# Kernel tuning notes

Measured on AMD Instinct MI355X. Metric: run time of the kernel, lower is better.

The kernel has to match this reference:

```python
import jax, jax.numpy as jnp
import numpy as np
import math

D_MODEL = 1024
N_HEADS = 16
D_HEAD = D_MODEL // N_HEADS
D_FF = 4 * D_MODEL
EPS = 1e-5


def layer_norm(x, gamma, beta):
    mu = jnp.mean(x, axis=-1, keepdims=True)
    var = jnp.var(x, axis=-1, keepdims=True)
    return (x - mu) * jax.lax.rsqrt(var + EPS) * gamma + beta


def setup_inputs() -> dict:
    key = jax.random.key(0)
    ks = jax.random.split(key, 8)
    B, C, D = 32, 256, D_MODEL
    s = 0.02
    return {
        "X": jax.random.normal(ks[0], (B, C, D), dtype=jnp.float32),
        "W_qkv": jax.random.normal(ks[1], (D, 3 * D), dtype=jnp.float32) * s,
        "b_qkv": jnp.zeros((3 * D,), dtype=jnp.float32),
        "W_proj": jax.random.normal(ks[2], (D, D), dtype=jnp.float32) * s,
        "b_proj": jnp.zeros((D,), dtype=jnp.float32),
        "g1": jnp.ones((D,), dtype=jnp.float32),
        "beta1": jnp.zeros((D,), dtype=jnp.float32),
        "g2": jnp.ones((D,), dtype=jnp.float32),
        "beta2": jnp.zeros((D,), dtype=jnp.float32),
        "W_ff1": jax.random.normal(ks[3], (D, D_FF), dtype=jnp.float32) * s,
        "b_ff1": jnp.zeros((D_FF,), dtype=jnp.float32),
        "W_ff2": jax.random.normal(ks[4], (D_FF, D), dtype=jnp.float32) * s,
        "b_ff2": jnp.zeros((D,), dtype=jnp.float32),
    }


def reference(X, W_qkv, b_qkv, W_proj, b_proj, g1, beta1, g2, beta2,
              W_ff1, b_ff1, W_ff2, b_ff2):
    B, C, D = X.shape
    H, Dh = N_HEADS, D_HEAD
    scale = 1.0 / math.sqrt(Dh)

    Xn = layer_norm(X, g1, beta1)
    qkv = Xn @ W_qkv + b_qkv                       # [B, C, 3D]
    q, k, v = jnp.split(qkv, 3, axis=-1)
    # split heads -> [B, H, C, Dh]
    sh = lambda t: t.reshape(B, C, H, Dh).transpose(0, 2, 1, 3)
    q, k, v = sh(q), sh(k), sh(v)

    scores = jnp.einsum("bhcd,bhkd->bhck", q, k) * scale  # [B, H, C, C]
    attn = jax.nn.softmax(scores, axis=-1)
    ctx = jnp.einsum("bhck,bhkd->bhcd", attn, v)           # [B, H, C, Dh]
    ctx = ctx.transpose(0, 2, 1, 3).reshape(B, C, D)

    X1 = X + (ctx @ W_proj + b_proj)
    X2n = layer_norm(X1, g2, beta2)
    h = jax.nn.gelu(X2n @ W_ff1 + b_ff1, approximate=False)
    X_out = X1 + (h @ W_ff2 + b_ff2)
    A = attn.mean(axis=1)                                   # [B, C, C]
    return (X_out, A)
```

## Files before the change

### kernel.cpp

```cpp
#include <hip/hip_runtime.h>
#include <cstdint>
#include <cstddef>

typedef short bf16x8 __attribute__((ext_vector_type(8)));
typedef float f32x4 __attribute__((ext_vector_type(4)));
typedef unsigned short u16;
typedef u16 u16x8 __attribute__((ext_vector_type(8)));

#define GLD16(gptr, lptr)                                                            \
  __builtin_amdgcn_global_load_lds((const __attribute__((address_space(1))) void*)(gptr), \
                                   (__attribute__((address_space(3))) void*)(lptr), 16, 0, 0)

__device__ __forceinline__ u16 f2bf(float f) {
  union { float f; unsigned u; } v; v.f = f;
  unsigned r = v.u + 0x7FFF + ((v.u >> 16) & 1);
  return (u16)(r >> 16);
}
__device__ __forceinline__ float bf2f(u16 h) {
  union { unsigned u; float f; } v; v.u = ((unsigned)h) << 16;
  return v.f;
}

__device__ __forceinline__ bf16x8 lds_read_sw64(const u16* base, int row, int col) {
  int byt = row * 128 + col * 2;
  byt ^= (row & 7) << 4;
  return *(const bf16x8*)((const char*)base + byt);
}

__global__ __launch_bounds__(256) void transpose_cast(const float* __restrict__ in,
                                                      u16* __restrict__ out, int R, int C) {
  __shared__ float tile[32][33];
  const int tx = threadIdx.x, ty = threadIdx.y;
  const int c0 = blockIdx.x * 32, r0 = blockIdx.y * 32;
#pragma unroll
  for (int i = 0; i < 32; i += 8)
    tile[ty + i][tx] = in[(size_t)(r0 + ty + i) * C + c0 + tx];
  __syncthreads();
#pragma unroll
  for (int i = 0; i < 32; i += 8)
    out[(size_t)(c0 + ty + i) * R + r0 + tx] = f2bf(tile[tx][ty + i]);
}

__global__ __launch_bounds__(256) void layernorm_bf16(const float* __restrict__ X,
                                                      const float* __restrict__ g,
                                                      const float* __restrict__ be,
                                                      u16* __restrict__ out) {
  const int row = blockIdx.x, t = threadIdx.x;
  const int lane = t & 63, wave = t >> 6;
  const float* x = X + (size_t)row * 1024;
  __shared__ float part[4];
  float v[4]; float s = 0.f;
#pragma unroll
  for (int i = 0; i < 4; ++i) { v[i] = x[t + i * 256]; s += v[i]; }
#pragma unroll
  for (int o = 32; o >= 1; o >>= 1) s += __shfl_xor(s, o);
  if (lane == 0) part[wave] = s;
  __syncthreads();
  const float mu = (part[0] + part[1] + part[2] + part[3]) * (1.f / 1024.f);
  float d2 = 0.f;
#pragma unroll
  for (int i = 0; i < 4; ++i) { float d = v[i] - mu; d2 += d * d; }
#pragma unroll
  for (int o = 32; o >= 1; o >>= 1) d2 += __shfl_xor(d2, o);
  __syncthreads();
  if (lane == 0) part[wave] = d2;
  __syncthreads();
  const float var = (part[0] + part[1] + part[2] + part[3]) * (1.f / 1024.f);
  const float rstd = rsqrtf(var + 1e-5f);
#pragma unroll
  for (int i = 0; i < 4; ++i) {
    const int c = t + i * 256;
    out[(size_t)row * 1024 + c] = f2bf((v[i] - mu) * rstd * g[c] + be[c]);
  }
}

template <int EPI, int WM, int WN, int BN>
__global__ __launch_bounds__(512, 2) void gemm_r2(const u16* __restrict__ A,
                                                  const u16* __restrict__ Bt,
                                                  const float* __restrict__ bias,
                                                  const float* __restrict__ res,
                                                  float* __restrict__ outf,
                                                  u16* __restrict__ outb,
                                                  int M, int N, int K) {
  constexpr int BM = 256;
  constexpr int WR = BM / WM, WC = BN / WN;
  constexpr int MF = WR / 16, NF = WC / 16;
  constexpr int ABYT = BM * 128, BBYT = BN * 128;
  constexpr int LA = BM / 64, LB = BN / 64;
  __shared__ __attribute__((aligned(16))) char lds[2 * (ABYT + BBYT)];

  const int t = threadIdx.x, lane = t & 63, wave = t >> 6;
  const int wm = wave / WN, wn = wave % WN;
  const int l15 = lane & 15, l16 = lane >> 4;

  const int lb = (blockIdx.x & 7) * ((int)gridDim.x >> 3) + ((int)blockIdx.x >> 3);
  const int NBN = N / BN;
  const int bm = (lb / NBN) * BM, bn = (lb % NBN) * BN;

  const u16* aptr[LA];
  const u16* bptr[LB];
#pragma unroll
  for (int c = 0; c < LA; ++c) {
    int Lb = c * 8192 + t * 16;
    int x = (Lb ^ ((Lb >> 3) & 0x70)) >> 1;
    aptr[c] = A + (size_t)(bm + (x >> 6)) * K + (x & 63);
  }
#pragma unroll
  for (int c = 0; c < LB; ++c) {
    int Lb = c * 8192 + t * 16;
    int x = (Lb ^ ((Lb >> 3) & 0x70)) >> 1;
    bptr[c] = Bt + (size_t)(bn + (x >> 6)) * K + (x & 63);
  }

  auto stage = [&](int p) {
    const int ko = p * 64;
    const int s = p & 1;
    char* ab = lds + s * ABYT + t * 16;
    char* bb = lds + 2 * ABYT + s * BBYT + t * 16;
#pragma unroll
    for (int c = 0; c < LA; ++c) GLD16(aptr[c] + ko, ab + c * 8192);
#pragma unroll
    for (int c = 0; c < LB; ++c) GLD16(bptr[c] + ko, bb + c * 8192);
  };
  stage(0);

  const int co0 = l16 * 16, co1 = 64 + l16 * 16;
  f32x4 acc[MF][NF] = {};
  const int nkt = K >> 6;

#pragma unroll 1
  for (int kt = 0; kt < nkt; ++kt) {
    asm volatile("s_waitcnt vmcnt(0)" ::: "memory");
    asm volatile("s_waitcnt lgkmcnt(0)" ::: "memory");
    asm volatile("s_barrier" ::: "memory");
    if (kt + 1 < nkt) stage(kt + 1);

    const int s = kt & 1;
    const char* ab = lds + s * ABYT;
    const char* bb = lds + 2 * ABYT + s * BBYT;
#pragma unroll
    for (int ks = 0; ks < 2; ++ks) {
      const int co = ks ? co1 : co0;
      bf16x8 a[MF], b[NF];
#pragma unroll
      for (int m = 0; m < MF; ++m) {
        const int r = wm * WR + m * 16 + l15;
        a[m] = *(const bf16x8*)(ab + r * 128 + (co ^ ((r & 7) << 4)));
      }
#pragma unroll
      for (int n = 0; n < NF; ++n) {
        const int r = wn * WC + n * 16 + l15;
        b[n] = *(const bf16x8*)(bb + r * 128 + (co ^ ((r & 7) << 4)));
      }
      __builtin_amdgcn_s_setprio(1);
#pragma unroll
      for (int m = 0; m < MF; ++m)
#pragma unroll
        for (int n = 0; n < NF; ++n)
          acc[m][n] = __builtin_amdgcn_mfma_f32_16x16x32_bf16(a[m], b[n], acc[m][n], 0, 0, 0);
      __builtin_amdgcn_s_setprio(0);
    }
  }

  const int r0 = l16 * 4;
#pragma unroll
  for (int m = 0; m < MF; ++m) {
#pragma unroll
    for (int n = 0; n < NF; ++n) {
      const int col = bn + wn * WC + n * 16 + l15;
      const float bv = bias[col];
#pragma unroll
      for (int r = 0; r < 4; ++r) {
        const int row = bm + wm * WR + m * 16 + r0 + r;
        const float v = acc[m][n][r] + bv;
        const size_t o = (size_t)row * N + col;
        if (EPI == 0) {
          outb[o] = f2bf(v);
        } else if (EPI == 1) {
          outf[o] = res[o] + v;
        } else {
          const float u = 0.7978845608f * (v + 0.044715f * v * v * v);
          const float e = __expf(2.f * u);
          const float th = 1.f - 2.f / (1.f + e);
          outb[o] = f2bf(0.5f * v * (1.f + th));
        }
      }
    }
  }
}

__global__ __launch_bounds__(256) void attn_scores(const u16* __restrict__ qkv,
                                                   u16* __restrict__ probs) {
  __shared__ u16 Ks[256 * 64];
  __shared__ u16 Qs[64 * 64];
  const int t = threadIdx.x, lane = t & 63, wave = t >> 6;
  const int qb = blockIdx.x * 64, h = blockIdx.y, b = blockIdx.z;
  const size_t row0 = (size_t)b * 256 * 3072;

#pragma unroll
  for (int is = 0; is < 8; ++is) {
    int L = (is * 2048 + t * 8) * 2;
    int x = (L ^ ((L >> 3) & 0x70)) >> 1;
    int kk = x >> 6, d = x & 63;
    const u16* gp = qkv + row0 + (size_t)kk * 3072 + 1024 + h * 64 + d;
    GLD16(gp, (char*)Ks + is * 4096 + wave * 1024);
  }
#pragma unroll
  for (int is = 0; is < 2; ++is) {
    int L = (is * 2048 + t * 8) * 2;
    int x = (L ^ ((L >> 3) & 0x70)) >> 1;
    int q = x >> 6, d = x & 63;
    const u16* gp = qkv + row0 + (size_t)(qb + q) * 3072 + h * 64 + d;
    GLD16(gp, (char*)Qs + is * 4096 + wave * 1024);
  }
  __syncthreads();

  f32x4 acc[16] = {};
  bf16x8 aq[2];
#pragma unroll
  for (int ks = 0; ks < 2; ++ks)
    aq[ks] = lds_read_sw64(Qs, wave * 16 + (lane & 15), ks * 32 + (lane >> 4) * 8);
#pragma unroll
  for (int nf = 0; nf < 16; ++nf) {
#pragma unroll
    for (int ks = 0; ks < 2; ++ks) {
      bf16x8 bk = lds_read_sw64(Ks, nf * 16 + (lane & 15), ks * 32 + (lane >> 4) * 8);
      acc[nf] = __builtin_amdgcn_mfma_f32_16x16x32_bf16(aq[ks], bk, acc[nf], 0, 0, 0);
    }
  }

  const int r0 = (lane >> 4) * 4, cc = lane & 15;
  const float sc = 0.125f;
#pragma unroll
  for (int r = 0; r < 4; ++r) {
    float mx = -1e30f;
#pragma unroll
    for (int nf = 0; nf < 16; ++nf) mx = fmaxf(mx, acc[nf][r]);
#pragma unroll
    for (int o = 8; o >= 1; o >>= 1) mx = fmaxf(mx, __shfl_xor(mx, o));
    float s = 0.f;
#pragma unroll
    for (int nf = 0; nf < 16; ++nf) {
      float e = __expf((acc[nf][r] - mx) * sc);
      acc[nf][r] = e; s += e;
    }
#pragma unroll
    for (int o = 8; o >= 1; o >>= 1) s += __shfl_xor(s, o);
    const float rinv = 1.f / s;
    const int qrow = qb + wave * 16 + r0 + r;
    u16* prow = probs + (size_t)((b * 16 + h) * 256 + qrow) * 256;
#pragma unroll
    for (int nf = 0; nf < 16; ++nf)
      prow[nf * 16 + cc] = f2bf(acc[nf][r] * rinv);
  }
}

__global__ __launch_bounds__(256) void amean(const u16* __restrict__ probs,
                                             float* __restrict__ A) {
  const int bq = blockIdx.x;
  const int b = bq >> 8, q = bq & 255;
  const int t = threadIdx.x;
  float s = 0.f;
#pragma unroll
  for (int h = 0; h < 16; ++h)
    s += bf2f(probs[(size_t)((b * 16 + h) * 256 + q) * 256 + t]);
  A[(size_t)bq * 256 + t] = s * (1.f / 16.f);
}

__global__ __launch_bounds__(256) void attn_pv(const u16* __restrict__ qkv,
                                               const u16* __restrict__ probs,
                                               u16* __restrict__ ctx) {
  __shared__ u16 Vs[64 * 256];
  const int t = threadIdx.x, lane = t & 63, wave = t >> 6;
  const int h = blockIdx.x, b = blockIdx.y;

#pragma unroll
  for (int p = 0; p < 8; ++p) {
    int idx = p * 2048 + t * 8;
    int kk = idx >> 6, d0 = idx & 63;
    u16x8 vv = *(const u16x8*)(qkv + (size_t)(b * 256 + kk) * 3072 + 2048 + h * 64 + d0);
#pragma unroll
    for (int j = 0; j < 8; ++j) {
      int d = d0 + j;
      int byt = (d * 512 + kk * 2) ^ ((d & 7) << 4);
      *(u16*)((char*)Vs + byt) = vv[j];
    }
  }
  __syncthreads();

  f32x4 acc[4][4] = {};
  const u16* Pb = probs + (size_t)((b * 16 + h) * 256) * 256;
  const int cc = lane & 15, kg = (lane >> 4) * 8;
#pragma unroll
  for (int kt = 0; kt < 8; ++kt) {
    bf16x8 a[4], v[4];
#pragma unroll
    for (int m = 0; m < 4; ++m)
      a[m] = *(const bf16x8*)(Pb + (size_t)(wave * 64 + m * 16 + cc) * 256 + kt * 32 + kg);
#pragma unroll
    for (int n = 0; n < 4; ++n) {
      int d = n * 16 + cc;
      int kk = kt * 32 + kg;
      int byt = (d * 512 + kk * 2) ^ ((d & 7) << 4);
      v[n] = *(const bf16x8*)((const char*)Vs + byt);
    }
#pragma unroll
    for (int m = 0; m < 4; ++m)
#pragma unroll
      for (int n = 0; n < 4; ++n)
        acc[m][n] = __builtin_amdgcn_mfma_f32_16x16x32_bf16(a[m], v[n], acc[m][n], 0, 0, 0);
  }

  const int r0 = (lane >> 4) * 4;
#pragma unroll
  for (int m = 0; m < 4; ++m) {
    const int q = wave * 64 + m * 16 + r0;
#pragma unroll
    for (int n = 0; n < 4; ++n) {
      const int col = h * 64 + n * 16 + cc;
#pragma unroll
      for (int r = 0; r < 4; ++r)
        ctx[(size_t)(b * 256 + q + r) * 1024 + col] = f2bf(acc[m][n][r]);
    }
  }
}

extern "C" void kernel_launch(void* const* d_in, const int* in_sizes, int n_in,
                              void* d_out, int out_size, void* d_ws, size_t ws_size,
                              hipStream_t stream) {
  const float* X      = (const float*)d_in[0];
  const float* W_qkv  = (const float*)d_in[1];
  const float* b_qkv  = (const float*)d_in[2];
  const float* W_proj = (const float*)d_in[3];
  const float* b_proj = (const float*)d_in[4];
  const float* g1     = (const float*)d_in[5];
  const float* beta1  = (const float*)d_in[6];
  const float* g2     = (const float*)d_in[7];
  const float* beta2  = (const float*)d_in[8];
  const float* W_ff1  = (const float*)d_in[9];
  const float* b_ff1  = (const float*)d_in[10];
  const float* W_ff2  = (const float*)d_in[11];
  const float* b_ff2  = (const float*)d_in[12];

  float* Xout = (float*)d_out;
  float* Aout = (float*)d_out + 8388608;

  char* ws = (char*)d_ws;
  const size_t MB = 1u << 20;
  u16* xn    = (u16*)(ws + 0);
  u16* wqkv  = (u16*)(ws + 16 * MB);
  u16* wproj = (u16*)(ws + 22 * MB);
  u16* wff1  = (u16*)(ws + 24 * MB);
  u16* wff2  = (u16*)(ws + 32 * MB);
  u16* qkv   = (u16*)(ws + 40 * MB);
  u16* probs = (u16*)(ws + 88 * MB);
  u16* hbuf  = probs;
  float* x1  = (float*)(ws + 152 * MB);
  u16* ctx   = xn;
  u16* x1n   = xn;

  const dim3 tb(32, 8);
  transpose_cast<<<dim3(96, 32),  tb, 0, stream>>>(W_qkv,  wqkv, 1024, 3072);
  transpose_cast<<<dim3(32, 32),  tb, 0, stream>>>(W_proj, wproj, 1024, 1024);
  transpose_cast<<<dim3(128, 32), tb, 0, stream>>>(W_ff1,  wff1, 1024, 4096);
  transpose_cast<<<dim3(32, 128), tb, 0, stream>>>(W_ff2,  wff2, 4096, 1024);

  layernorm_bf16<<<8192, 256, 0, stream>>>(X, g1, beta1, xn);

  gemm_r2<0, 2, 4, 256><<<384, 512, 0, stream>>>(xn, wqkv, b_qkv, nullptr, nullptr, qkv,
                                                 8192, 3072, 1024);

  attn_scores<<<dim3(4, 16, 32), 256, 0, stream>>>(qkv, probs);
  amean<<<8192, 256, 0, stream>>>(probs, Aout);
  attn_pv<<<dim3(16, 32), 256, 0, stream>>>(qkv, probs, ctx);

  gemm_r2<1, 4, 2, 128><<<256, 512, 0, stream>>>(ctx, wproj, b_proj, X, x1, nullptr,
                                                 8192, 1024, 1024);

  layernorm_bf16<<<8192, 256, 0, stream>>>(x1, g2, beta2, x1n);

  gemm_r2<2, 2, 4, 256><<<512, 512, 0, stream>>>(x1n, wff1, b_ff1, nullptr, nullptr, hbuf,
                                                 8192, 4096, 1024);

  gemm_r2<1, 4, 2, 128><<<256, 512, 0, stream>>>(hbuf, wff2, b_ff2, x1, Xout, nullptr,
                                                 8192, 1024, 4096);
}
```

Measured before the change: 354.4 us.

## Triple-buffer GEMM K-loop with BK=32 and smaller tiles for N=1024 GEMMs

Replaces the double-buffered, BK=64 GEMM with a templated version that uses three LDS stages of BK=32. It prefetches two stages ahead and waits with a partial vmcnt instead of draining all loads each iteration. The LDS layout packs two 32-wide K halves of rows into each 128-byte line, with an XOR swizzle. The projection and FF2 GEMMs move to 128x128 tiles with 256 threads so more blocks run. The intent is to hide global-load latency behind MFMA work. The cost is more barriers per K and half as many MFMAs between syncs.

Measured after the change: 369.8 us. +4.3%, slower.

```diff
diff --git a/kernel.cpp b/kernel.cpp
--- a/kernel.cpp
+++ b/kernel.cpp
@@ -74,92 +74,85 @@
   }
 }
 
-template <int EPI, int WM, int WN, int BN>
-__global__ __launch_bounds__(512, 2) void gemm_r2(const u16* __restrict__ A,
-                                                  const u16* __restrict__ Bt,
-                                                  const float* __restrict__ bias,
-                                                  const float* __restrict__ res,
-                                                  float* __restrict__ outf,
-                                                  u16* __restrict__ outb,
-                                                  int M, int N, int K) {
-  constexpr int BM = 256;
+template <int EPI, int BM, int BN, int TPB, int WM, int WN>
+__global__ __launch_bounds__(TPB) void gemm_p(const u16* __restrict__ A,
+                                              const u16* __restrict__ Bt,
+                                              const float* __restrict__ bias,
+                                              const float* __restrict__ res,
+                                              float* __restrict__ outf,
+                                              u16* __restrict__ outb,
+                                              int M, int N, int K) {
   constexpr int WR = BM / WM, WC = BN / WN;
   constexpr int MF = WR / 16, NF = WC / 16;
-  constexpr int ABYT = BM * 128, BBYT = BN * 128;
-  constexpr int LA = BM / 64, LB = BN / 64;
-  __shared__ __attribute__((aligned(16))) char lds[2 * (ABYT + BBYT)];
+  constexpr int ASZ = BM * 64, BSZ = BN * 64;
+  constexpr int NLD = (BM * 64) / (TPB * 16);
+  __shared__ __attribute__((aligned(16))) char lds[3 * (ASZ + BSZ)];
 
   const int t = threadIdx.x, lane = t & 63, wave = t >> 6;
   const int wm = wave / WN, wn = wave % WN;
   const int l15 = lane & 15, l16 = lane >> 4;
 
-  const int lb = (blockIdx.x & 7) * ((int)gridDim.x >> 3) + ((int)blockIdx.x >> 3);
+  const int lb = ((int)blockIdx.x & 7) * ((int)gridDim.x >> 3) + ((int)blockIdx.x >> 3);
   const int NBN = N / BN;
   const int bm = (lb / NBN) * BM, bn = (lb % NBN) * BN;
 
-  const u16* aptr[LA];
-  const u16* bptr[LB];
-#pragma unroll
-  for (int c = 0; c < LA; ++c) {
-    int Lb = c * 8192 + t * 16;
-    int x = (Lb ^ ((Lb >> 3) & 0x70)) >> 1;
-    aptr[c] = A + (size_t)(bm + (x >> 6)) * K + (x & 63);
-  }
-#pragma unroll
-  for (int c = 0; c < LB; ++c) {
-    int Lb = c * 8192 + t * 16;
-    int x = (Lb ^ ((Lb >> 3) & 0x70)) >> 1;
-    bptr[c] = Bt + (size_t)(bn + (x >> 6)) * K + (x & 63);
+  const u16* aptr[NLD];
+  const u16* bptr[NLD];
+#pragma unroll
+  for (int c = 0; c < NLD; ++c) {
+    const int d = c * TPB * 16 + t * 16;
+    const int r2 = d >> 7;
+    const int sl = ((d >> 4) & 7) ^ (r2 & 7);
+    aptr[c] = A + (size_t)(bm + r2 + (sl >> 2) * (BM / 2)) * K + (sl & 3) * 8;
+    bptr[c] = Bt + (size_t)(bn + r2 + (sl >> 2) * (BN / 2)) * K + (sl & 3) * 8;
   }
 
   auto stage = [&](int p) {
-    const int ko = p * 64;
-    const int s = p & 1;
-    char* ab = lds + s * ABYT + t * 16;
-    char* bb = lds + 2 * ABYT + s * BBYT + t * 16;
-#pragma unroll
-    for (int c = 0; c < LA; ++c) GLD16(aptr[c] + ko, ab + c * 8192);
-#pragma unroll
-    for (int c = 0; c < LB; ++c) GLD16(bptr[c] + ko, bb + c * 8192);
+    const int ko = p * 32;
+    const int s = p % 3;
+    char* ab = lds + s * ASZ + t * 16;
+    char* bb = lds + 3 * ASZ + s * BSZ + t * 16;
+#pragma unroll
+    for (int c = 0; c < NLD; ++c) GLD16(aptr[c] + ko, ab + c * TPB * 16);
+#pragma unroll
+    for (int c = 0; c < NLD; ++c) GLD16(bptr[c] + ko, bb + c * TPB * 16);
   };
-  stage(0);
-
-  const int co0 = l16 * 16, co1 = 64 + l16 * 16;
+  stage(0); stage(1);
+
+  const int sw = (l15 & 7) << 4;
+  const int acol = (wm * 64 + l16 * 16) ^ sw;
+  constexpr int HB = BN / 2;
+  const int hiB = (wn * WC) / HB;
+  const int fB0 = (wn * WC) % HB;
+  const int bcol = (hiB * 64 + l16 * 16) ^ sw;
+
   f32x4 acc[MF][NF] = {};
-  const int nkt = K >> 6;
+  const int nkt = K >> 5;
 
 #pragma unroll 1
   for (int kt = 0; kt < nkt; ++kt) {
-    asm volatile("s_waitcnt vmcnt(0)" ::: "memory");
-    asm volatile("s_waitcnt lgkmcnt(0)" ::: "memory");
+    if (kt < nkt - 1) asm volatile("s_waitcnt vmcnt(4)" ::: "memory");
+    else              asm volatile("s_waitcnt vmcnt(0)" ::: "memory");
     asm volatile("s_barrier" ::: "memory");
-    if (kt + 1 < nkt) stage(kt + 1);
-
-    const int s = kt & 1;
-    const char* ab = lds + s * ABYT;
-    const char* bb = lds + 2 * ABYT + s * BBYT;
-#pragma unroll
-    for (int ks = 0; ks < 2; ++ks) {
-      const int co = ks ? co1 : co0;
-      bf16x8 a[MF], b[NF];
-#pragma unroll
-      for (int m = 0; m < MF; ++m) {
-        const int r = wm * WR + m * 16 + l15;
-        a[m] = *(const bf16x8*)(ab + r * 128 + (co ^ ((r & 7) << 4)));
-      }
-#pragma unroll
-      for (int n = 0; n < NF; ++n) {
-        const int r = wn * WC + n * 16 + l15;
-        b[n] = *(const bf16x8*)(bb + r * 128 + (co ^ ((r & 7) << 4)));
-      }
-      __builtin_amdgcn_s_setprio(1);
-#pragma unroll
-      for (int m = 0; m < MF; ++m)
-#pragma unroll
-        for (int n = 0; n < NF; ++n)
-          acc[m][n] = __builtin_amdgcn_mfma_f32_16x16x32_bf16(a[m], b[n], acc[m][n], 0, 0, 0);
-      __builtin_amdgcn_s_setprio(0);
-    }
+    if (kt + 2 < nkt) stage(kt + 2);
+
+    const int s = kt % 3;
+    const char* ab = lds + s * ASZ;
+    const char* bb = lds + 3 * ASZ + s * BSZ;
+    bf16x8 a[MF], b[NF];
+#pragma unroll
+    for (int m = 0; m < MF; ++m)
+      a[m] = *(const bf16x8*)(ab + (m * 16 + l15) * 128 + acol);
+#pragma unroll
+    for (int n = 0; n < NF; ++n)
+      b[n] = *(const bf16x8*)(bb + (fB0 + n * 16 + l15) * 128 + bcol);
+    __builtin_amdgcn_s_setprio(1);
+#pragma unroll
+    for (int m = 0; m < MF; ++m)
+#pragma unroll
+      for (int n = 0; n < NF; ++n)
+        acc[m][n] = __builtin_amdgcn_mfma_f32_16x16x32_bf16(a[m], b[n], acc[m][n], 0, 0, 0);
+    __builtin_amdgcn_s_setprio(0);
   }
 
   const int r0 = l16 * 4;
@@ -367,21 +360,21 @@
 
   layernorm_bf16<<<8192, 256, 0, stream>>>(X, g1, beta1, xn);
 
-  gemm_r2<0, 2, 4, 256><<<384, 512, 0, stream>>>(xn, wqkv, b_qkv, nullptr, nullptr, qkv,
-                                                 8192, 3072, 1024);
+  gemm_p<0, 256, 256, 512, 2, 4><<<384, 512, 0, stream>>>(
+      xn, wqkv, b_qkv, nullptr, nullptr, qkv, 8192, 3072, 1024);
 
   attn_scores<<<dim3(4, 16, 32), 256, 0, stream>>>(qkv, probs);
   amean<<<8192, 256, 0, stream>>>(probs, Aout);
   attn_pv<<<dim3(16, 32), 256, 0, stream>>>(qkv, probs, ctx);
 
-  gemm_r2<1, 4, 2, 128><<<256, 512, 0, stream>>>(ctx, wproj, b_proj, X, x1, nullptr,
-                                                 8192, 1024, 1024);
+  gemm_p<1, 128, 128, 256, 2, 2><<<512, 256, 0, stream>>>(
+      ctx, wproj, b_proj, X, x1, nullptr, 8192, 1024, 1024);
 
   layernorm_bf16<<<8192, 256, 0, stream>>>(x1, g2, beta2, x1n);
 
-  gemm_r2<2, 2, 4, 256><<<512, 512, 0, stream>>>(x1n, wff1, b_ff1, nullptr, nullptr, hbuf,
-                                                 8192, 4096, 1024);
-
-  gemm_r2<1, 4, 2, 128><<<256, 512, 0, stream>>>(hbuf, wff2, b_ff2, x1, Xout, nullptr,
-                                                 8192, 1024, 4096);
-}
+  gemm_p<2, 256, 256, 512, 2, 4><<<512, 512, 0, stream>>>(
+      x1n, wff1, b_ff1, nullptr, nullptr, hbuf, 8192, 4096, 1024);
+
+  gemm_p<1, 128, 128, 256, 2, 2><<<512, 256, 0, stream>>>(
+      hbuf, wff2, b_ff2, x1, Xout, nullptr, 8192, 1024, 4096);
+}
```
